# Performance work log

Measured on AMD Instinct MI355X. Metric: run time of the kernel, lower is better.

The kernel has to match this reference:

```python
import jax, jax.numpy as jnp
import numpy as np

IN_CH, OUT_CH, L, INTERVAL = 128, 128, 80, 5
NCPT = int(np.ceil(L / INTERVAL)) + 1            # 17 anchor points
INTERVAL2 = 1 if INTERVAL == 1 else L - (NCPT - 2) * INTERVAL  # 5
P = (L + 1) ** 2                                  # 6561 positions
# static repeat_interleave index: degree l occupies 2l+1 positions
REPEAT_IDX = np.repeat(np.arange(L + 1), 2 * np.arange(L + 1) + 1)  # [P]


def setup_inputs() -> dict:
    key = jax.random.key(0)
    kx, kw = jax.random.split(key)
    x = jax.random.normal(kx, (16, IN_CH, P), dtype=jnp.float32)
    stdv = 1.0 / float(np.sqrt(IN_CH * (L + 1)))
    weight = jax.random.uniform(kw, (IN_CH, OUT_CH, NCPT, 1), dtype=jnp.float32,
                                minval=-stdv, maxval=stdv)
    return {"x": x, "weight": weight}


def _interp_filter(weight):
    # weight: [in, out, ncpt, 1] -> per-degree coeffs [in, out, L+1]
    w = weight[..., 0]                                   # [in, out, ncpt]
    l0 = jnp.arange(INTERVAL, dtype=w.dtype) / INTERVAL  # [interval]
    # segments between anchors 0..ncpt-2: [in, out, ncpt-2, interval]
    w1 = (1.0 - l0) * w[:, :, :-2, None] + l0 * w[:, :, 1:-1, None]
    w1 = w1.reshape(w.shape[0], w.shape[1], -1)          # [in, out, (ncpt-2)*interval]
    l1 = jnp.arange(INTERVAL2 + 1, dtype=w.dtype) / INTERVAL2  # [interval2+1]
    w2 = (1.0 - l1) * w[:, :, -2, None] + l1 * w[:, :, -1, None]  # [in, out, interval2+1]
    wl = jnp.concatenate([w1, w2], axis=2)               # [in, out, L+1]
    return wl[:, :, REPEAT_IDX]                          # [in, out, P]


def reference(x, weight):
    wp = _interp_filter(weight)                          # [in, out, P]
    # out[b,o,p] = sum_i wp[i,o,p] * x[b,i,p]  (fused, no [b,in,out,P] temp)
    return jnp.einsum('iop,bip->bop', wp, x)
```

## Files before the change

### kernel.cpp

```cpp
#include <hip/hip_runtime.h>

#define IC    128
#define OC    128
#define NL    81
#define PTOT  6561
#define NCPT  17
#define BSTR  (IC*PTOT)
#define NBLK  1681

typedef short short8 __attribute__((ext_vector_type(8)));
typedef float f32x4  __attribute__((ext_vector_type(4)));

__device__ __forceinline__ unsigned short f2bf(float x) {
    unsigned u = __float_as_uint(x);
    return (unsigned short)((u + 0x7FFFu + ((u >> 16) & 1u)) >> 16);
}

__global__ __launch_bounds__(256) void shconv_prep(const float* __restrict__ w,
                                                   unsigned short* __restrict__ WtF) {
    const int l    = blockIdx.x >> 2;
    const int quad = blockIdx.x & 3;
    int s; float fr;
    if (l < 75) { s = l / 5;  fr = (float)(l - s * 5) * 0.2f; }
    else        { s = 15;     fr = (float)(l - 75) * 0.2f;    }
    unsigned short* dst = WtF + (size_t)l * (OC * IC);
    const int e0 = quad * 4096;
    for (int e = e0 + threadIdx.x; e < e0 + 4096; e += 256) {
        int j  = e & 7;
        int mm = (e >> 3) & 15;
        int gg = (e >> 7) & 3;
        int kk = (e >> 9) & 3;
        int of = e >> 11;
        int o = of * 16 + mm;
        int i = kk * 32 + gg * 8 + j;
        const float* wp = w + i * (OC * NCPT) + o * NCPT + s;
        float v = (1.0f - fr) * wp[0] + fr * wp[1];
        dst[e] = f2bf(v);
    }
}

__global__ __launch_bounds__(256, 4) void shconv_main(const float* __restrict__ x,
                                                      const unsigned short* __restrict__ WtF,
                                                      float* __restrict__ out) {
    const int tid = threadIdx.x;

    int q = blockIdx.x;
    int t = (int)sqrtf((float)q);
    while (t * t > q) --t;
    while ((t + 1) * (t + 1) <= q) ++t;
    int l, chunk;
    if (q < t * (t + 1)) { l = 2 * t - 1; chunk = q - t * t; }
    else                 { l = 2 * t;     chunk = q - t * (t + 1); }

    const int len  = 2 * l + 1;
    const int cols = 16 * len;
    const int c0   = chunk * 64;

    const int lane = tid & 63;
    const int wave = tid >> 6;
    const int m    = lane & 15;
    const int g    = lane >> 4;

    int c = c0 + wave * 16 + m;
    const bool valid = (c < cols);
    int ccl = valid ? c : (cols - 1);
    int b   = (int)((unsigned)ccl / (unsigned)len);
    int pp  = ccl - b * len;
    int p   = l * l + pp;

    const float* xg = x + (size_t)b * BSTR + (size_t)(g * 8) * PTOT + p;
    const unsigned short* wf = WtF + (size_t)l * (OC * IC) + (size_t)lane * 8;

    float xv[32];
    #pragma unroll
    for (int kk = 0; kk < 4; ++kk)
        #pragma unroll
        for (int j = 0; j < 8; ++j)
            xv[kk * 8 + j] = xg[(kk * 32 + j) * PTOT];
    __builtin_amdgcn_sched_barrier(0);

    short8 bfr[4];
    #pragma unroll
    for (int kk = 0; kk < 4; ++kk)
        #pragma unroll
        for (int j = 0; j < 8; ++j)
            bfr[kk][j] = (short)f2bf(xv[kk * 8 + j]);

    f32x4 acc[8];
    #pragma unroll
    for (int of = 0; of < 8; ++of) acc[of] = (f32x4){0.f, 0.f, 0.f, 0.f};

    #pragma unroll
    for (int kk = 0; kk < 4; ++kk) {
        short8 af[8];
        #pragma unroll
        for (int of = 0; of < 8; ++of)
            af[of] = *(const short8*)(wf + (size_t)(of * 4 + kk) * 512);
        #pragma unroll
        for (int of = 0; of < 8; ++of)
            acc[of] = __builtin_amdgcn_mfma_f32_16x16x32_bf16(af[of], bfr[kk], acc[of], 0, 0, 0);
    }

    if (valid) {
        float* ob = out + (size_t)b * (OC * PTOT) + p;
        #pragma unroll
        for (int of = 0; of < 8; ++of)
            #pragma unroll
            for (int j = 0; j < 4; ++j)
                ob[(of * 16 + g * 4 + j) * PTOT] = acc[of][j];
    }
}

extern "C" void kernel_launch(void* const* d_in, const int* in_sizes, int n_in,
                              void* d_out, int out_size, void* d_ws, size_t ws_size,
                              hipStream_t stream) {
    const float* x = (const float*)d_in[0];
    const float* w = (const float*)d_in[1];
    unsigned short* WtF = (unsigned short*)d_ws;
    float* out = (float*)d_out;

    shconv_prep<<<dim3(NL * 4), dim3(256), 0, stream>>>(w, WtF);
    shconv_main<<<dim3(NBLK),   dim3(256), 0, stream>>>(x, WtF, out);
}
```

Measured before the change: 132.6 us.

## Retile main kernel per batch and degree with 4-wide position vectors per lane

Reorganises the work split so each block handles one batch and one degree (or half of a high degree), covering up to 128 positions. Each lane now loads 4 contiguous positions of x per channel, which gives wider coalesced reads, and each wave computes a 64-output by 64-position tile. Every weight fragment is reused across 4 MFMAs. Rows are aligned down to a multiple of 4 and masked at the degree boundaries, so some neighbouring positions are loaded redundantly. Register use rises, so occupancy is lowered to 2 waves per SIMD.

Measured after the change: 139.8 us. +5.4%, slower.

```diff
diff --git a/kernel.cpp b/kernel.cpp
--- a/kernel.cpp
+++ b/kernel.cpp
@@ -6,7 +6,7 @@
 #define PTOT  6561
 #define NCPT  17
 #define BSTR  (IC*PTOT)
-#define NBLK  1681
+#define NBLK  1568
 
 typedef short short8 __attribute__((ext_vector_type(8)));
 typedef float f32x4  __attribute__((ext_vector_type(4)));
@@ -39,75 +39,83 @@
     }
 }
 
-__global__ __launch_bounds__(256, 4) void shconv_main(const float* __restrict__ x,
+__global__ __launch_bounds__(256, 2) void shconv_main(const float* __restrict__ x,
                                                       const unsigned short* __restrict__ WtF,
                                                       float* __restrict__ out) {
-    const int tid = threadIdx.x;
+    const int bid = blockIdx.x;
+    const int b   = bid / 98;
+    const int r   = bid - b * 98;
+    int l, chunk;
+    if (r < 64) { l = r; chunk = 0; }
+    else        { int rr = r - 64; l = 64 + (rr >> 1); chunk = rr & 1; }
 
-    int q = blockIdx.x;
-    int t = (int)sqrtf((float)q);
-    while (t * t > q) --t;
-    while ((t + 1) * (t + 1) <= q) ++t;
-    int l, chunk;
-    if (q < t * (t + 1)) { l = 2 * t - 1; chunk = q - t * t; }
-    else                 { l = 2 * t;     chunk = q - t * (t + 1); }
+    const int p2     = l * l;
+    const int len    = 2 * l + 1;
+    const int pstart = p2 & ~3;
 
-    const int len  = 2 * l + 1;
-    const int cols = 16 * len;
-    const int c0   = chunk * 64;
-
+    const int tid  = threadIdx.x;
+    const int wave = tid >> 6;
     const int lane = tid & 63;
-    const int wave = tid >> 6;
     const int m    = lane & 15;
     const int g    = lane >> 4;
+    const int nh   = wave & 1;
+    const int mh   = wave >> 1;
 
-    int c = c0 + wave * 16 + m;
-    const bool valid = (c < cols);
-    int ccl = valid ? c : (cols - 1);
-    int b   = (int)((unsigned)ccl / (unsigned)len);
-    int pp  = ccl - b * len;
-    int p   = l * l + pp;
+    const int pcol = pstart + chunk * 128 + nh * 64 + 4 * m;
+    int pr = pcol; if (pr > PTOT - 4) pr = PTOT - 4;
 
-    const float* xg = x + (size_t)b * BSTR + (size_t)(g * 8) * PTOT + p;
-    const unsigned short* wf = WtF + (size_t)l * (OC * IC) + (size_t)lane * 8;
+    const float* xg = x + (size_t)b * BSTR + (size_t)(g * 8) * PTOT + pr;
+    const unsigned short* wf = WtF + (size_t)l * (OC * IC) + (size_t)mh * 8192
+                                   + (size_t)lane * 8;
 
-    float xv[32];
+    f32x4 acc[4][4];
     #pragma unroll
-    for (int kk = 0; kk < 4; ++kk)
+    for (int of = 0; of < 4; ++of)
         #pragma unroll
-        for (int j = 0; j < 8; ++j)
-            xv[kk * 8 + j] = xg[(kk * 32 + j) * PTOT];
-    __builtin_amdgcn_sched_barrier(0);
-
-    short8 bfr[4];
-    #pragma unroll
-    for (int kk = 0; kk < 4; ++kk)
-        #pragma unroll
-        for (int j = 0; j < 8; ++j)
-            bfr[kk][j] = (short)f2bf(xv[kk * 8 + j]);
-
-    f32x4 acc[8];
-    #pragma unroll
-    for (int of = 0; of < 8; ++of) acc[of] = (f32x4){0.f, 0.f, 0.f, 0.f};
+        for (int d = 0; d < 4; ++d) acc[of][d] = (f32x4){0.f, 0.f, 0.f, 0.f};
 
     #pragma unroll
     for (int kk = 0; kk < 4; ++kk) {
-        short8 af[8];
+        float v[8][4];
         #pragma unroll
-        for (int of = 0; of < 8; ++of)
-            af[of] = *(const short8*)(wf + (size_t)(of * 4 + kk) * 512);
+        for (int j = 0; j < 8; ++j)
+            #pragma unroll
+            for (int d = 0; d < 4; ++d)
+                v[j][d] = xg[(size_t)(kk * 32 + j) * PTOT + d];
+
+        short8 bfr[4];
         #pragma unroll
-        for (int of = 0; of < 8; ++of)
-            acc[of] = __builtin_amdgcn_mfma_f32_16x16x32_bf16(af[of], bfr[kk], acc[of], 0, 0, 0);
+        for (int d = 0; d < 4; ++d)
+            #pragma unroll
+            for (int j = 0; j < 8; ++j)
+                bfr[d][j] = (short)f2bf(v[j][d]);
+
+        short8 af[4];
+        #pragma unroll
+        for (int of = 0; of < 4; ++of)
+            af[of] = *(const short8*)(wf + ((size_t)(of * 4 + kk) << 9));
+
+        #pragma unroll
+        for (int of = 0; of < 4; ++of)
+            #pragma unroll
+            for (int d = 0; d < 4; ++d)
+                acc[of][d] = __builtin_amdgcn_mfma_f32_16x16x32_bf16(af[of], bfr[d], acc[of][d], 0, 0, 0);
     }
 
-    if (valid) {
-        float* ob = out + (size_t)b * (OC * PTOT) + p;
+    float* ob0 = out + (size_t)b * (OC * PTOT);
+    const int phi = p2 + len;
+    #pragma unroll
+    for (int of = 0; of < 4; ++of) {
+        const int obase = (mh * 4 + of) * 16 + g * 4;
         #pragma unroll
-        for (int of = 0; of < 8; ++of)
+        for (int j = 0; j < 4; ++j) {
+            float* ob = ob0 + (size_t)(obase + j) * PTOT;
             #pragma unroll
-            for (int j = 0; j < 4; ++j)
-                ob[(of * 16 + g * 4 + j) * PTOT] = acc[of][j];
+            for (int d = 0; d < 4; ++d) {
+                int p = pr + d;
+                if (p >= p2 && p < phi) ob[p] = acc[of][d][j];
+            }
+        }
     }
 }
 
```
